# Kernel optimization log

Hardware: AMD Instinct MI355X
Metric: run time of the kernel (lower is better)

The kernel has to match this reference:

```python
import jax, jax.numpy as jnp
import numpy as np

NUM_HEADS = 16
ROPE_BASE = 10000.0


def _rope_cache(seq_len, head_dim, base, dtype):
    inv_freq = 1.0 / (base ** (jnp.arange(0, head_dim, 2, dtype=jnp.float32) / head_dim))
    t = jnp.arange(seq_len, dtype=jnp.float32)
    freqs = jnp.outer(t, inv_freq)                      # [S, D/2]
    emb = jnp.concatenate([freqs, freqs], axis=-1)      # [S, D]
    return jnp.cos(emb).astype(dtype), jnp.sin(emb).astype(dtype)


def _rotate_half(x):
    half = x.shape[-1] // 2
    return jnp.concatenate([-x[..., half:], x[..., :half]], axis=-1)


def _apply_rope(x, cos, sin):
    # x: [B, H, S, D]; cos/sin: [S, D]
    return x * cos[None, None] + _rotate_half(x) * sin[None, None]


def setup_inputs() -> dict:
    key = jax.random.key(0)
    ks = jax.random.split(key, 5)
    B, S, Dm = 2, 2048, 1024
    hidden_states = jax.random.normal(ks[0], (B, S, Dm), dtype=jnp.float32)
    attention_mask = jnp.ones((B, S), dtype=bool)
    scale = 1.0 / np.sqrt(Dm)
    Wq = jax.random.normal(ks[1], (Dm, Dm), dtype=jnp.float32) * scale
    Wk = jax.random.normal(ks[2], (Dm, Dm), dtype=jnp.float32) * scale
    Wv = jax.random.normal(ks[3], (Dm, Dm), dtype=jnp.float32) * scale
    Wo = jax.random.normal(ks[4], (Dm, Dm), dtype=jnp.float32) * scale
    return {"hidden_states": hidden_states, "attention_mask": attention_mask,
            "Wq": Wq, "Wk": Wk, "Wv": Wv, "Wo": Wo}


def reference(hidden_states, attention_mask, Wq, Wk, Wv, Wo):
    B, S, Dm = hidden_states.shape
    H = NUM_HEADS
    D = Dm // H

    def to_heads(x):
        return x.reshape(B, S, H, D).transpose(0, 2, 1, 3)  # [B, H, S, D]

    q = to_heads(hidden_states @ Wq.T)
    k = to_heads(hidden_states @ Wk.T)
    v = to_heads(hidden_states @ Wv.T)

    cos, sin = _rope_cache(S, D, ROPE_BASE, hidden_states.dtype)
    q = _apply_rope(q, cos, sin)
    k = _apply_rope(k, cos, sin)

    scores = jnp.einsum('bhqd,bhkd->bhqk', q, k) / jnp.sqrt(jnp.array(D, hidden_states.dtype))
    key_mask = attention_mask[:, None, None, :]  # [B,1,1,S]
    min_val = jnp.finfo(scores.dtype).min
    scores = jnp.where(key_mask, scores, min_val)

    weights = jax.nn.softmax(scores.astype(jnp.float32), axis=-1).astype(hidden_states.dtype)
    context = jnp.einsum('bhqk,bhkd->bhqd', weights, v)
    context = context.transpose(0, 2, 1, 3).reshape(B, S, Dm)
    return context @ Wo.T
```

## Files before the change

kernel.cpp:

```cpp
#include <hip/hip_runtime.h>
#include <math.h>


typedef __bf16 bf16_t;
typedef __bf16 bf16x8 __attribute__((ext_vector_type(8)));
typedef __bf16 bf16x4 __attribute__((ext_vector_type(4)));
typedef float f32x4 __attribute__((ext_vector_type(4)));
typedef float f32x16 __attribute__((ext_vector_type(16)));

#define AS1 __attribute__((address_space(1)))
#define AS3 __attribute__((address_space(3)))

#define SCALE_Q 0.18033688011112042f

__device__ __forceinline__ void gld_lds16(const bf16_t* g, bf16_t* l) {
  __builtin_amdgcn_global_load_lds((const AS1 unsigned int*)(const void*)g,
                                   (AS3 unsigned int*)(void*)l, 16, 0, 0);
}

__global__ void rope_table_k(float* __restrict__ cost, float* __restrict__ sint, int n) {
  int i = blockIdx.x * blockDim.x + threadIdx.x;
  if (i >= n) return;
  int j = i & 31, s = i >> 5;
  float invf = powf(10000.0f, -(float)j * (1.0f / 32.0f));
  float a = (float)s * invf;
  cost[i] = cosf(a);
  sint[i] = sinf(a);
}

__global__ void cvt_f32_bf16(const float* __restrict__ in, bf16_t* __restrict__ out, int n4) {
  int i = blockIdx.x * blockDim.x + threadIdx.x;
  if (i >= n4) return;
  float4 v = ((const float4*)in)[i];
  bf16x4 o = {(bf16_t)v.x, (bf16_t)v.y, (bf16_t)v.z, (bf16_t)v.w};
  ((bf16x4*)out)[i] = o;
}

__global__ void cvt4_w(const float* __restrict__ a, const float* __restrict__ b,
                       const float* __restrict__ c, const float* __restrict__ d,
                       bf16_t* __restrict__ out) {
  int i = blockIdx.x * blockDim.x + threadIdx.x;
  const float* src = blockIdx.y == 0 ? a : blockIdx.y == 1 ? b : blockIdx.y == 2 ? c : d;
  float4 v = ((const float4*)src)[i];
  bf16x4 o = {(bf16_t)v.x, (bf16_t)v.y, (bf16_t)v.z, (bf16_t)v.w};
  ((bf16x4*)(out + (size_t)blockIdx.y * 1048576))[i] = o;
}


#define GEMM_STAGE(buf, k0)                                                     \
  {                                                                             \
    _Pragma("unroll") for (int c = 0; c < 4; ++c) {                             \
      const int rg = wid * 4 + c;                                               \
      const int r = rg * 8 + sr8;                                               \
      const int key = (sr8 + rg) & 7;                                           \
      const int sc = (scol ^ key) << 3;                 \
      const int dst = rg * 1024 + (lane << 4);                                  \
      gld_lds16(A + (size_t)(brow + r) * 1024 + (k0) + sc,                      \
                (bf16_t*)((char*)&As[buf][0] + dst));                           \
      gld_lds16(Bt + (size_t)(bcol + r) * 1024 + (k0) + sc,                     \
                (bf16_t*)((char*)&Bs[buf][0] + dst));                           \
    }                                                                           \
  }

#define GEMM_COMPUTE(cur)                                                       \
  {                                                                             \
    _Pragma("unroll") for (int kk = 0; kk < 2; ++kk) {                          \
      bf16x8 af[4], bfr[4];                                                     \
      _Pragma("unroll") for (int mm = 0; mm < 4; ++mm) {                        \
        const int keyA = ((lr & 7) + (lr >> 3) + 2 * mm) & 7;                   \
        af[mm] = *(const bf16x8*)((const char*)&As[cur][0] +                    \
                                  (wr * 64 + mm * 16 + lr) * 128 +              \
                                  ((kk * 64 + lg * 16) ^ (keyA << 4)));         \
      }                                                                         \
      _Pragma("unroll") for (int nn = 0; nn < 4; ++nn) {                        \
        const int keyB = ((lr & 7) + (lr >> 3) + 2 * nn) & 7;                   \
        bfr[nn] = *(const bf16x8*)((const char*)&Bs[cur][0] +                   \
                                   (wc * 64 + nn * 16 + lr) * 128 +             \
                                   ((kk * 64 + lg * 16) ^ (keyB << 4)));        \
      }                                                                         \
      _Pragma("unroll") for (int mm = 0; mm < 4; ++mm)                          \
          _Pragma("unroll") for (int nn = 0; nn < 4; ++nn) acc[mm][nn] =        \
          __builtin_amdgcn_mfma_f32_16x16x32_bf16(af[mm], bfr[nn],              \
                                                  acc[mm][nn], 0, 0, 0);        \
    }                                                                           \
  }

__global__ __launch_bounds__(256) void qkv_gemm(const bf16_t* __restrict__ Aall,
                                                const bf16_t* __restrict__ Wq,
                                                const bf16_t* __restrict__ Wk,
                                                const bf16_t* __restrict__ Wv,
                                                bf16_t* __restrict__ Qr,
                                                bf16_t* __restrict__ Kr,
                                                bf16_t* __restrict__ Vtr,
                                                const float* __restrict__ cost,
                                                const float* __restrict__ sint) {
  __shared__ bf16_t As[2][128 * 64];
  __shared__ bf16_t Bs[2][128 * 64];
  int lid = blockIdx.y * 24 + blockIdx.x;
  lid = (lid & 7) * 96 + (lid >> 3);
  const int bx = lid % 24, by = lid / 24;
  const int which = bx >> 3;
  const int bcol = (bx & 7) * 128;
  const int brow = by * 128;
  const bf16_t* A = Aall;
  const bf16_t* Bt = which == 0 ? Wq : which == 1 ? Wk : Wv;

  const int tid = threadIdx.x;
  const int wid = tid >> 6, lane = tid & 63;
  const int lr = lane & 15, lg = lane >> 4;
  const int wr = wid >> 1, wc = wid & 1;
  const int sr8 = lane >> 3, scol = lane & 7;

  f32x4 acc[4][4];
#pragma unroll
  for (int m = 0; m < 4; ++m)
#pragma unroll
    for (int n = 0; n < 4; ++n) acc[m][n] = (f32x4){0.f, 0.f, 0.f, 0.f};

  GEMM_STAGE(0, 0)
  __syncthreads();
  for (int kt = 0; kt < 16; ++kt) {
    const int cur = kt & 1;
    if (kt < 15) GEMM_STAGE(cur ^ 1, (kt + 1) * 64)
    GEMM_COMPUTE(cur)
    __syncthreads();
  }

  if (which == 2) {
#pragma unroll
    for (int m = 0; m < 4; ++m)
#pragma unroll
      for (int n = 0; n < 4; ++n) {
        int row = brow + wr * 64 + m * 16 + lg * 4;
        int col = bcol + wc * 64 + n * 16 + lr;
        int b = row >> 11, s = row & 2047;
        int lgp = ((lg & 1) << 1) | (lg >> 1);
        int sp = s - lg * 4 + lgp * 4;
        bf16x4 pack = {(bf16_t)acc[m][n][0], (bf16_t)acc[m][n][1], (bf16_t)acc[m][n][2],
                       (bf16_t)acc[m][n][3]};
        *(bf16x4*)&Vtr[((size_t)(b * 1024 + col) << 11) + sp] = pack;
      }
  } else {
    bf16_t* C = which == 0 ? Qr : Kr;
    float scale = which == 0 ? SCALE_Q : 1.0f;
#pragma unroll
    for (int m = 0; m < 4; ++m)
#pragma unroll
      for (int n = 0; n < 2; ++n) {
        int row = brow + wr * 64 + m * 16 + lg * 4;
        int col = bcol + wc * 64 + n * 16 + lr;
        int j = n * 16 + lr;
#pragma unroll
        for (int r = 0; r < 4; ++r) {
          int s = (row + r) & 2047;
          float c = cost[s * 32 + j], sn = sint[s * 32 + j];
          float x0 = acc[m][n][r], x1 = acc[m][n + 2][r];
          C[(size_t)(row + r) * 1024 + col] = (bf16_t)((x0 * c - x1 * sn) * scale);
          C[(size_t)(row + r) * 1024 + col + 32] = (bf16_t)((x1 * c + x0 * sn) * scale);
        }
      }
  }
}

__global__ __launch_bounds__(256) void out_gemm(const bf16_t* __restrict__ A,
                                                const bf16_t* __restrict__ Bt,
                                                float* __restrict__ C) {
  __shared__ bf16_t As[2][128 * 64];
  __shared__ bf16_t Bs[2][128 * 64];
  int lid = blockIdx.y * 8 + blockIdx.x;
  lid = (lid & 7) * 32 + (lid >> 3);
  const int bcol = (lid & 7) * 128;
  const int brow = (lid >> 3) * 128;

  const int tid = threadIdx.x;
  const int wid = tid >> 6, lane = tid & 63;
  const int lr = lane & 15, lg = lane >> 4;
  const int wr = wid >> 1, wc = wid & 1;
  const int sr8 = lane >> 3, scol = lane & 7;

  f32x4 acc[4][4];
#pragma unroll
  for (int m = 0; m < 4; ++m)
#pragma unroll
    for (int n = 0; n < 4; ++n) acc[m][n] = (f32x4){0.f, 0.f, 0.f, 0.f};

  GEMM_STAGE(0, 0)
  __syncthreads();
  for (int kt = 0; kt < 16; ++kt) {
    const int cur = kt & 1;
    if (kt < 15) GEMM_STAGE(cur ^ 1, (kt + 1) * 64)
    GEMM_COMPUTE(cur)
    __syncthreads();
  }

#pragma unroll
  for (int m = 0; m < 4; ++m)
#pragma unroll
    for (int n = 0; n < 4; ++n) {
      int row = brow + wr * 64 + m * 16 + lg * 4;
      int col = bcol + wc * 64 + n * 16 + lr;
#pragma unroll
      for (int r = 0; r < 4; ++r) C[(size_t)(row + r) * 1024 + col] = acc[m][n][r];
    }
}

__global__ __launch_bounds__(128, 2) void attn_k(const bf16_t* __restrict__ Q,
                                                 const bf16_t* __restrict__ K,
                                                 const bf16_t* __restrict__ Vt,
                                                 bf16_t* __restrict__ ctx) {
  const int S = 2048, HD = 1024;
  int lid = blockIdx.y * 32 + blockIdx.x;
  lid = (lid & 7) * 128 + (lid >> 3);
  const int bh = lid >> 5, bx = lid & 31;
  const int b = bh >> 4, h = bh & 15;
  const int wid = threadIdx.x >> 6, lane = threadIdx.x & 63;
  const int lq = lane & 31, hi = lane >> 5;
  const int q0 = bx * 64 + wid * 32;

  const bf16_t* Qb = Q + (size_t)b * S * HD + h * 64;
  const bf16_t* Kb = K + (size_t)b * S * HD + h * 64;
  const bf16_t* Vb = Vt + (size_t)bh * 64 * S;

  __shared__ bf16_t KL[2][64 * 64];
  __shared__ bf16_t VL[2][64 * 64];

  bf16x8 qf[4];
#pragma unroll
  for (int d0 = 0; d0 < 4; ++d0)
    qf[d0] = *(const bf16x8*)&Qb[(size_t)(q0 + lq) * HD + d0 * 16 + hi * 8];

  f32x16 o0 = (f32x16)0.0f, o1 = (f32x16)0.0f, osum = (f32x16)0.0f;

  bf16x8 ones;
#pragma unroll
  for (int j = 0; j < 8; ++j) ones[j] = (bf16_t)1.0f;

  const int sr = lane >> 3, sc7 = lane & 7;

#define STAGE(buf, s0)                                                          \
  if (wid == 0) {                                                               \
    _Pragma("unroll") for (int c = 0; c < 8; ++c) {                             \
      gld_lds16((const bf16_t*)((const char*)Kb +                               \
                                (size_t)((s0) + c * 8 + sr) * 2048 +            \
                                ((sc7 ^ ((sr + c) & 7)) << 4)),                 \
                (bf16_t*)((char*)&KL[buf][0] + c * 1024 + lane * 16));          \
    }                                                                           \
  } else {                                                                      \
    _Pragma("unroll") for (int c = 0; c < 8; ++c) {                             \
      gld_lds16((const bf16_t*)((const char*)Vb +                               \
                                (size_t)(c * 8 + sr) * 4096 +                   \
                                (size_t)(s0) * 2 +                              \
                                ((sc7 ^ ((sr + c) & 7)) << 4)),                 \
                (bf16_t*)((char*)&VL[buf][0] + c * 1024 + lane * 16));          \
    }                                                                           \
  }

  STAGE(0, 0)
  __syncthreads();

  const int keyLo = ((lq & 7) + (lq >> 3)) & 7;
  const int keyHi = (keyLo + 4) & 7;

  for (int t = 0; t < 32; ++t) {
    const int cur = t & 1;
    if (t + 1 < 32) STAGE(cur ^ 1, (t + 1) * 64)

    bf16x8 kc0[4], kc1[4], vb0[4], vb1[4];
#pragma unroll
    for (int d0 = 0; d0 < 4; ++d0) {
      const int base = d0 * 32 + hi * 16;
      const int wlo = base ^ (keyLo << 4), whi = base ^ (keyHi << 4);
      kc0[d0] = *(const bf16x8*)((const char*)&KL[cur][0] + lq * 128 + wlo);
      kc1[d0] = *(const bf16x8*)((const char*)&KL[cur][0] + (32 + lq) * 128 + whi);
      vb0[d0] = *(const bf16x8*)((const char*)&VL[cur][0] + lq * 128 + wlo);
      vb1[d0] = *(const bf16x8*)((const char*)&VL[cur][0] + (32 + lq) * 128 + whi);
    }
    f32x16 st0 = (f32x16)0.0f, st1 = (f32x16)0.0f;
    __builtin_amdgcn_s_setprio(1);
#pragma unroll
    for (int d0 = 0; d0 < 4; ++d0) {
      st0 = __builtin_amdgcn_mfma_f32_32x32x16_bf16(kc0[d0], qf[d0], st0, 0, 0, 0);
      st1 = __builtin_amdgcn_mfma_f32_32x32x16_bf16(kc1[d0], qf[d0], st1, 0, 0, 0);
    }
    __builtin_amdgcn_s_setprio(0);
#pragma unroll
    for (int r = 0; r < 16; ++r) {
      st0[r] = __builtin_amdgcn_exp2f(st0[r]);
      st1[r] = __builtin_amdgcn_exp2f(st1[r]);
    }
    bf16x8 pa[4];
#pragma unroll
    for (int j = 0; j < 8; ++j) {
      pa[0][j] = (bf16_t)st0[j];
      pa[1][j] = (bf16_t)st0[8 + j];
      pa[2][j] = (bf16_t)st1[j];
      pa[3][j] = (bf16_t)st1[8 + j];
    }
    __builtin_amdgcn_s_setprio(1);
#pragma unroll
    for (int ks = 0; ks < 4; ++ks) {
      o0 = __builtin_amdgcn_mfma_f32_32x32x16_bf16(pa[ks], vb0[ks], o0, 0, 0, 0);
      o1 = __builtin_amdgcn_mfma_f32_32x32x16_bf16(pa[ks], vb1[ks], o1, 0, 0, 0);
      osum = __builtin_amdgcn_mfma_f32_32x32x16_bf16(pa[ks], ones, osum, 0, 0, 0);
    }
    __builtin_amdgcn_s_setprio(0);
    __syncthreads();
  }
  bf16_t* cb = ctx + ((size_t)b * S + q0) * HD + h * 64 + lq;
#pragma unroll
  for (int r = 0; r < 16; ++r) {
    int qr = (r & 3) + 8 * (r >> 2) + 4 * hi;
    float nf = 1.0f / osum[r];
    cb[(size_t)qr * HD] = (bf16_t)(o0[r] * nf);
    cb[(size_t)qr * HD + 32] = (bf16_t)(o1[r] * nf);
  }
#undef STAGE
}

extern "C" void kernel_launch(void* const* d_in, const int* in_sizes, int n_in,
                              void* d_out, int out_size, void* d_ws, size_t ws_size,
                              hipStream_t stream) {
  const float* hs = (const float*)d_in[0];
  const float* Wq = (const float*)d_in[2];
  const float* Wk = (const float*)d_in[3];
  const float* Wv = (const float*)d_in[4];
  const float* Wo = (const float*)d_in[5];
  float* out = (float*)d_out;

  const int S = 2048, Dm = 1024;
  const int M = 2 * S;

  char* p = (char*)d_ws;
  auto alloc = [&](size_t bytes) {
    char* q = p;
    p += (bytes + 255) & ~(size_t)255;
    return q;
  };
  float* cost = (float*)alloc((size_t)S * 32 * 4);
  float* sint = (float*)alloc((size_t)S * 32 * 4);
  bf16_t* hsb = (bf16_t*)alloc((size_t)M * Dm * 2);
  bf16_t* Wb = (bf16_t*)alloc((size_t)4 * Dm * Dm * 2);
  bf16_t* Wqb = Wb;
  bf16_t* Wkb = Wb + (size_t)Dm * Dm;
  bf16_t* Wvb = Wb + (size_t)2 * Dm * Dm;
  bf16_t* Wob = Wb + (size_t)3 * Dm * Dm;
  bf16_t* Qr = (bf16_t*)alloc((size_t)M * Dm * 2);
  bf16_t* Kr = (bf16_t*)alloc((size_t)M * Dm * 2);
  bf16_t* Vtr = (bf16_t*)alloc((size_t)M * Dm * 2);
  bf16_t* ctx = (bf16_t*)alloc((size_t)M * Dm * 2);

  rope_table_k<<<(S * 32 + 255) / 256, 256, 0, stream>>>(cost, sint, S * 32);
  cvt_f32_bf16<<<(M * Dm / 4 + 255) / 256, 256, 0, stream>>>(hs, hsb, M * Dm / 4);
  cvt4_w<<<dim3(Dm * Dm / 4 / 256, 4), 256, 0, stream>>>(Wq, Wk, Wv, Wo, Wb);

  qkv_gemm<<<dim3(24, 32), 256, 0, stream>>>(hsb, Wqb, Wkb, Wvb, Qr, Kr, Vtr, cost, sint);

  attn_k<<<dim3(32, 32), 128, 0, stream>>>(Qr, Kr, Vtr, ctx);

  out_gemm<<<dim3(8, 32), 256, 0, stream>>>(ctx, Wob, out);
}
```

Before: 137.5 us.

## Load K fragments directly into registers with double buffering, stage only V via LDS

The attention kernel stops staging K tiles through shared memory. Each lane now loads its K rows straight from global memory into registers, one tile ahead, ping-ponging between two register sets across a loop unrolled by two. V staging is split across both waves instead of one wave per tensor, and the LDS footprint is halved. The aim is to cut LDS traffic and shrink shared memory per block. The cost is higher register pressure, redundant per-wave global K reads, and a wasted wraparound prefetch on the last iteration.

```diff
diff --git a/kernel.cpp b/kernel.cpp
--- a/kernel.cpp
+++ b/kernel.cpp
@@ -221,7 +221,6 @@
   const bf16_t* Kb = K + (size_t)b * S * HD + h * 64;
   const bf16_t* Vb = Vt + (size_t)bh * 64 * S;
 
-  __shared__ bf16_t KL[2][64 * 64];
   __shared__ bf16_t VL[2][64 * 64];
 
   bf16x8 qf[4];
@@ -235,77 +234,84 @@
 #pragma unroll
   for (int j = 0; j < 8; ++j) ones[j] = (bf16_t)1.0f;
 
+  const bf16_t* krow0 = Kb + (size_t)lq * HD + hi * 8;
+  const bf16_t* krow1 = Kb + (size_t)(32 + lq) * HD + hi * 8;
+
   const int sr = lane >> 3, sc7 = lane & 7;
 
-#define STAGE(buf, s0)                                                          \
-  if (wid == 0) {                                                               \
-    _Pragma("unroll") for (int c = 0; c < 8; ++c) {                             \
-      gld_lds16((const bf16_t*)((const char*)Kb +                               \
-                                (size_t)((s0) + c * 8 + sr) * 2048 +            \
-                                ((sc7 ^ ((sr + c) & 7)) << 4)),                 \
-                (bf16_t*)((char*)&KL[buf][0] + c * 1024 + lane * 16));          \
-    }                                                                           \
-  } else {                                                                      \
-    _Pragma("unroll") for (int c = 0; c < 8; ++c) {                             \
-      gld_lds16((const bf16_t*)((const char*)Vb +                               \
-                                (size_t)(c * 8 + sr) * 4096 +                   \
-                                (size_t)(s0) * 2 +                              \
-                                ((sc7 ^ ((sr + c) & 7)) << 4)),                 \
-                (bf16_t*)((char*)&VL[buf][0] + c * 1024 + lane * 16));          \
-    }                                                                           \
-  }
-
-  STAGE(0, 0)
+#define VSTAGE(buf, s0)                                                         \
+  {                                                                             \
+    _Pragma("unroll") for (int c = 0; c < 4; ++c) {                             \
+      const int cc = wid * 4 + c;                                               \
+      gld_lds16((const bf16_t*)((const char*)Vb + (size_t)(cc * 8 + sr) * 4096 +\
+                                (size_t)(s0) * 2 + ((sc7 ^ ((sr + cc) & 7)) << 4)), \
+                (bf16_t*)((char*)&VL[buf][0] + cc * 1024 + lane * 16));         \
+    }                                                                           \
+  }
+
+#define KLOAD(dst0, dst1, s0)                                                   \
+  {                                                                             \
+    _Pragma("unroll") for (int d0 = 0; d0 < 4; ++d0) {                          \
+      dst0[d0] = *(const bf16x8*)&krow0[(size_t)(s0) * HD + d0 * 16];           \
+      dst1[d0] = *(const bf16x8*)&krow1[(size_t)(s0) * HD + d0 * 16];           \
+    }                                                                           \
+  }
+
+  bf16x8 kA0[4], kA1[4], kB0[4], kB1[4];
+  KLOAD(kA0, kA1, 0)
+  VSTAGE(0, 0)
   __syncthreads();
 
   const int keyLo = ((lq & 7) + (lq >> 3)) & 7;
   const int keyHi = (keyLo + 4) & 7;
 
-  for (int t = 0; t < 32; ++t) {
-    const int cur = t & 1;
-    if (t + 1 < 32) STAGE(cur ^ 1, (t + 1) * 64)
-
-    bf16x8 kc0[4], kc1[4], vb0[4], vb1[4];
-#pragma unroll
-    for (int d0 = 0; d0 < 4; ++d0) {
-      const int base = d0 * 32 + hi * 16;
-      const int wlo = base ^ (keyLo << 4), whi = base ^ (keyHi << 4);
-      kc0[d0] = *(const bf16x8*)((const char*)&KL[cur][0] + lq * 128 + wlo);
-      kc1[d0] = *(const bf16x8*)((const char*)&KL[cur][0] + (32 + lq) * 128 + whi);
-      vb0[d0] = *(const bf16x8*)((const char*)&VL[cur][0] + lq * 128 + wlo);
-      vb1[d0] = *(const bf16x8*)((const char*)&VL[cur][0] + (32 + lq) * 128 + whi);
-    }
-    f32x16 st0 = (f32x16)0.0f, st1 = (f32x16)0.0f;
-    __builtin_amdgcn_s_setprio(1);
-#pragma unroll
-    for (int d0 = 0; d0 < 4; ++d0) {
-      st0 = __builtin_amdgcn_mfma_f32_32x32x16_bf16(kc0[d0], qf[d0], st0, 0, 0, 0);
-      st1 = __builtin_amdgcn_mfma_f32_32x32x16_bf16(kc1[d0], qf[d0], st1, 0, 0, 0);
-    }
-    __builtin_amdgcn_s_setprio(0);
-#pragma unroll
-    for (int r = 0; r < 16; ++r) {
-      st0[r] = __builtin_amdgcn_exp2f(st0[r]);
-      st1[r] = __builtin_amdgcn_exp2f(st1[r]);
-    }
-    bf16x8 pa[4];
-#pragma unroll
-    for (int j = 0; j < 8; ++j) {
-      pa[0][j] = (bf16_t)st0[j];
-      pa[1][j] = (bf16_t)st0[8 + j];
-      pa[2][j] = (bf16_t)st1[j];
-      pa[3][j] = (bf16_t)st1[8 + j];
-    }
-    __builtin_amdgcn_s_setprio(1);
-#pragma unroll
-    for (int ks = 0; ks < 4; ++ks) {
-      o0 = __builtin_amdgcn_mfma_f32_32x32x16_bf16(pa[ks], vb0[ks], o0, 0, 0, 0);
-      o1 = __builtin_amdgcn_mfma_f32_32x32x16_bf16(pa[ks], vb1[ks], o1, 0, 0, 0);
-      osum = __builtin_amdgcn_mfma_f32_32x32x16_bf16(pa[ks], ones, osum, 0, 0, 0);
-    }
-    __builtin_amdgcn_s_setprio(0);
-    __syncthreads();
-  }
+#define ATTN_ITER(t, kc0, kc1, kn0, kn1)                                        \
+  {                                                                             \
+    const int cur = (t) & 1;                                                    \
+    const int s2 = (((t) + 1) & 31) * 64;                                       \
+    VSTAGE(cur ^ 1, s2)                                                         \
+    KLOAD(kn0, kn1, s2)                                                         \
+    bf16x8 vb0[4], vb1[4];                                                      \
+    _Pragma("unroll") for (int d0 = 0; d0 < 4; ++d0) {                          \
+      const int base = d0 * 32 + hi * 16;                                       \
+      vb0[d0] = *(const bf16x8*)((const char*)&VL[cur][0] + lq * 128 +          \
+                                 (base ^ (keyLo << 4)));                        \
+      vb1[d0] = *(const bf16x8*)((const char*)&VL[cur][0] + (32 + lq) * 128 +   \
+                                 (base ^ (keyHi << 4)));                        \
+    }                                                                           \
+    f32x16 st0 = (f32x16)0.0f, st1 = (f32x16)0.0f;                              \
+    __builtin_amdgcn_s_setprio(1);                                              \
+    _Pragma("unroll") for (int d0 = 0; d0 < 4; ++d0) {                          \
+      st0 = __builtin_amdgcn_mfma_f32_32x32x16_bf16(kc0[d0], qf[d0], st0, 0, 0, 0); \
+      st1 = __builtin_amdgcn_mfma_f32_32x32x16_bf16(kc1[d0], qf[d0], st1, 0, 0, 0); \
+    }                                                                           \
+    __builtin_amdgcn_s_setprio(0);                                              \
+    _Pragma("unroll") for (int r = 0; r < 16; ++r) {                            \
+      st0[r] = __builtin_amdgcn_exp2f(st0[r]);                                  \
+      st1[r] = __builtin_amdgcn_exp2f(st1[r]);                                  \
+    }                                                                           \
+    bf16x8 pa[4];                                                               \
+    _Pragma("unroll") for (int j = 0; j < 8; ++j) {                             \
+      pa[0][j] = (bf16_t)st0[j];                                                \
+      pa[1][j] = (bf16_t)st0[8 + j];                                            \
+      pa[2][j] = (bf16_t)st1[j];                                                \
+      pa[3][j] = (bf16_t)st1[8 + j];                                            \
+    }                                                                           \
+    __builtin_amdgcn_s_setprio(1);                                              \
+    _Pragma("unroll") for (int ks = 0; ks < 4; ++ks) {                          \
+      o0 = __builtin_amdgcn_mfma_f32_32x32x16_bf16(pa[ks], vb0[ks], o0, 0, 0, 0); \
+      o1 = __builtin_amdgcn_mfma_f32_32x32x16_bf16(pa[ks], vb1[ks], o1, 0, 0, 0); \
+      osum = __builtin_amdgcn_mfma_f32_32x32x16_bf16(pa[ks], ones, osum, 0, 0, 0); \
+    }                                                                           \
+    __builtin_amdgcn_s_setprio(0);                                              \
+    __syncthreads();                                                            \
+  }
+
+  for (int tt = 0; tt < 16; ++tt) {
+    ATTN_ITER(2 * tt, kA0, kA1, kB0, kB1)
+    ATTN_ITER(2 * tt + 1, kB0, kB1, kA0, kA1)
+  }
+
   bf16_t* cb = ctx + ((size_t)b * S + q0) * HD + h * 64 + lq;
 #pragma unroll
   for (int r = 0; r < 16; ++r) {
@@ -314,7 +320,9 @@
     cb[(size_t)qr * HD] = (bf16_t)(o0[r] * nf);
     cb[(size_t)qr * HD + 32] = (bf16_t)(o1[r] * nf);
   }
-#undef STAGE
+#undef ATTN_ITER
+#undef KLOAD
+#undef VSTAGE
 }
 
 extern "C" void kernel_launch(void* const* d_in, const int* in_sizes, int n_in,
```

After: 158.0 us. +14.9%, slower.
